# Performance work log

Hardware: AMD Instinct MI355X
Metric: run time of the kernel (lower is better)

## Reference

```python
import jax, jax.numpy as jnp
import numpy as np

B, C, H, W = 16, 256, 64, 64
NH, DH = 8, 64
POS_C = 4


def setup_inputs() -> dict:
    key = jax.random.key(0)
    ks = jax.random.split(key, 10)
    cin = C + POS_C
    dqkv = NH * DH
    sc = 1.0 / np.sqrt(cin)
    inp = {
        "x": jax.random.normal(ks[0], (B, C, H, W), dtype=jnp.float32),
        "pos_emb": jax.random.normal(ks[1], (1, POS_C, H, W), dtype=jnp.float32) / np.sqrt(C * H * W),
        "Wk": jax.random.normal(ks[2], (dqkv, cin), dtype=jnp.float32) * sc,
        "bk": jnp.zeros((dqkv,), dtype=jnp.float32),
        "Wq": jax.random.normal(ks[3], (dqkv, cin), dtype=jnp.float32) * sc,
        "bq": jnp.zeros((dqkv,), dtype=jnp.float32),
        "Wv": jax.random.normal(ks[4], (dqkv, cin), dtype=jnp.float32) * sc,
        "bv": jnp.zeros((dqkv,), dtype=jnp.float32),
        "Wo": jax.random.normal(ks[5], (C, dqkv), dtype=jnp.float32) / np.sqrt(dqkv),
        "bo": jnp.zeros((C,), dtype=jnp.float32),
    }
    return inp


def _conv1x1(w, b, x):
    # w: (out, in), x: (B, in, H, W) -> (B, out, H, W)
    return jnp.einsum('oc,bchw->bohw', w, x) + b[None, :, None, None]


def reference(x, pos_emb, Wk, bk, Wq, bq, Wv, bv, Wo, bo):
    b, c, h, w = x.shape
    xp = jnp.concatenate([x, jnp.broadcast_to(pos_emb, (b, POS_C, h, w))], axis=1)
    K = _conv1x1(Wk, bk, xp).reshape(b, NH, DH, h, w)
    Q = _conv1x1(Wq, bq, xp).reshape(b, NH, DH, h, w)
    V = _conv1x1(Wv, bv, xp).reshape(b, NH, DH, h, w)
    # Row (width-axis) logits: (B, nh, H, W, W)
    qk_w = jnp.einsum('bhdij,bhdik->bhijk', Q, K)
    # Column (height-axis) logits: (B, nh, H, W, H)
    qk_h = jnp.einsum('bhdij,bhdkj->bhijk', Q, K)
    scale = 1.0 / np.sqrt(w + h)
    p = jax.nn.softmax(jnp.concatenate([qk_w, qk_h], axis=-1) * scale, axis=-1)
    p_w, p_h = p[..., :w], p[..., w:]
    a_w = jnp.einsum('bhijk,bhdik->bhdij', p_w, V)
    a_h = jnp.einsum('bhijk,bhdkj->bhdij', p_h, V)
    A = (a_w + a_h).reshape(b, NH * DH, h, w)
    return x + _conv1x1(Wo, bo, A)
```

## Files before the change

### kernel.cpp

```cpp
#include <hip/hip_runtime.h>

typedef unsigned short u16;
typedef __bf16 bf16x8 __attribute__((ext_vector_type(8)));
typedef float f32x4 __attribute__((ext_vector_type(4)));
typedef unsigned short u16x8 __attribute__((ext_vector_type(8)));
typedef unsigned short u16x4 __attribute__((ext_vector_type(4)));

#define MFMA16(A,B,C) __builtin_amdgcn_mfma_f32_16x16x32_bf16(A,B,C,0,0,0)

__device__ __forceinline__ float b2f(u16 h){ unsigned u = ((unsigned)h)<<16; return __builtin_bit_cast(float,u); }
__device__ __forceinline__ u16 f2b(float f){ unsigned u = __builtin_bit_cast(unsigned,f); u += 0x7fffu + ((u>>16)&1u); return (u16)(u>>16); }
__device__ __forceinline__ bf16x8 ldb8(const u16* p){ return __builtin_bit_cast(bf16x8, *(const u16x8*)p); }

__device__ __forceinline__ void g2lds16(const u16* g, u16* l){
  __builtin_amdgcn_global_load_lds((const __attribute__((address_space(1))) void*)g,
                                   (__attribute__((address_space(3))) void*)l, 16, 0, 0);
}


__global__ void k_prep_w(const float* __restrict__ Wq, const float* __restrict__ Wk,
                         const float* __restrict__ Wv, const float* __restrict__ bq,
                         const float* __restrict__ bk, const float* __restrict__ bv,
                         const float* __restrict__ Wo,
                         u16* __restrict__ WP, u16* __restrict__ WPOS,
                         u16* __restrict__ BIAS, u16* __restrict__ WoP){
  int r = blockIdx.x;
  int tid = threadIdx.x;
  if (r < 1536){
    int t = r >> 9, rm = r & 511;
    const float* src = (t==0 ? Wq : (t==1 ? Wk : Wv)) + (long)rm*260;
    WP[(long)r*256 + tid] = f2b(src[tid]);
    if (tid < 4) WPOS[r*4 + tid] = f2b(src[256 + tid]);
    if (tid == 0){
      const float* bs = (t==0 ? bq : (t==1 ? bk : bv));
      BIAS[r] = f2b(bs[rm]);
    }
  } else {
    int co = r - 1536;
    WoP[(long)co*512 + tid]       = f2b(Wo[(long)co*512 + tid]);
    WoP[(long)co*512 + 256 + tid] = f2b(Wo[(long)co*512 + 256 + tid]);
  }
}

__global__ void k_sentinel(float* __restrict__ out){
  long i = (long)blockIdx.x*256 + threadIdx.x;
  out[i] = 100.0f;
}

__global__ __launch_bounds__(256) void k_cvtx(const float* __restrict__ x,
                                              u16* __restrict__ XT, int b0){
  __shared__ u16 tile[64*65];
  int bidx = blockIdx.x;
  int ct = bidx & 3, pt = (bidx>>2)&63, bl = bidx>>8;
  int c0 = ct*64, p0 = pt*64;
  int tid = threadIdx.x;
  const float* xb = x + (long)(b0+bl)*256*4096;
  #pragma unroll
  for (int it=0; it<16; ++it){
    int idx = it*256 + tid; int cc = idx>>6, px = idx&63;
    tile[cc*65 + px] = f2b(xb[(long)(c0+cc)*4096 + p0 + px]);
  }
  __syncthreads();
  u16* dst = XT + ((long)(bl*4096 + p0))*256 + c0;
  #pragma unroll
  for (int it=0; it<4; ++it){
    int idx = it*256 + tid; int pp = idx>>4, c4 = (idx&15)*4;
    u16x4 o;
    #pragma unroll
    for (int u=0;u<4;++u) o[u] = tile[(c4+u)*65 + pp];
    *(u16x4*)&dst[(long)pp*256 + c4] = o;
  }
}

__global__ __launch_bounds__(256) void k_qkv(
    const u16* __restrict__ XT, const u16* __restrict__ WP,
    const u16* __restrict__ WPOS, const float* __restrict__ pos,
    const u16* __restrict__ BIAS,
    u16* __restrict__ Qb, u16* __restrict__ Kb, u16* __restrict__ Vt){
  __shared__ u16 sW[128*32];
  __shared__ u16 sX[128*32];
  __shared__ u16 sPW[512];
  __shared__ u16 sPP[512];
  int bidx = blockIdx.x;
  int mt = bidx % 12; long nt = bidx / 12;
  int oc0 = mt*128; long p0 = nt*128;
  int bl = (int)(p0>>12); int pl0 = (int)(p0 & 4095);
  int tid = threadIdx.x;
  for (int k = tid; k < 512; k += 256) sPW[k] = WPOS[(long)oc0*4 + k];
  for (int k = tid; k < 512; k += 256){ int c = k>>7, p = k&127; sPP[k] = f2b(pos[(long)c*4096 + pl0 + p]); }
  f32x4 zf = {0.f,0.f,0.f,0.f};
  f32x4 acc[4][4];
  #pragma unroll
  for (int i=0;i<4;++i){
    #pragma unroll
    for (int j=0;j<4;++j) acc[i][j] = zf;
  }
  int wid = tid>>6, lane = tid&63, l16 = lane&15, qd = lane>>4;
  int wm = wid>>1, wn = wid&1;
  int srow = lane>>2, sc8 = (lane&3)*8;
  for (int kk = 0; kk < 256; kk += 32){
    __syncthreads();
    #pragma unroll
    for (int c=0;c<2;++c){
      int seg = wid*2 + c;
      int row = seg*16 + srow;
      g2lds16(&WP[(long)(oc0+row)*256 + kk + sc8], &sW[seg*512]);
      g2lds16(&XT[(p0 + row)*256 + kk + sc8],      &sX[seg*512]);
    }
    __syncthreads();
    bf16x8 a[4], bb[4];
    #pragma unroll
    for (int mi=0;mi<4;++mi) a[mi]  = ldb8(&sW[(wm*64+mi*16+l16)*32 + qd*8]);
    #pragma unroll
    for (int ni=0;ni<4;++ni) bb[ni] = ldb8(&sX[(wn*64+ni*16+l16)*32 + qd*8]);
    #pragma unroll
    for (int mi=0;mi<4;++mi){
      #pragma unroll
      for (int ni=0;ni<4;++ni)
        acc[mi][ni] = MFMA16(a[mi], bb[ni], acc[mi][ni]);
    }
  }
  #pragma unroll
  for (int mi=0;mi<4;++mi){
    int mbase = wm*64 + mi*16 + qd*4;
    int ocb = oc0 + mbase;
    int t = ocb>>9, ocm = ocb&511;
    int hh = ocm>>6, dd = ocm&63;
    #pragma unroll
    for (int ni=0;ni<4;++ni){
      int n = wn*64 + ni*16 + l16;
      int pl = pl0 + n;
      float pv[4];
      #pragma unroll
      for (int r=0;r<4;++r){
        float v = acc[mi][ni][r];
        #pragma unroll
        for (int c=0;c<4;++c) v += b2f(sPW[(mbase+r)*4+c]) * b2f(sPP[c*128 + n]);
        pv[r] = v + b2f(BIAS[ocb + r]);
      }
      if (t < 2){
        u16* dstb = (t==0? Qb : Kb);
        u16x4 pk;
        #pragma unroll
        for (int r=0;r<4;++r) pk[r] = f2b(pv[r]);
        *(u16x4*)&dstb[((long)(bl*8+hh)*4096 + pl)*64 + dd] = pk;
      } else {
        long base = (long)(bl*8+hh)*262144 + (long)dd*4096 + pl;
        #pragma unroll
        for (int r=0;r<4;++r) Vt[base + (long)r*4096] = f2b(pv[r]);
      }
    }
  }
}

__global__ __launch_bounds__(256) void k_vtr(const u16* __restrict__ Vt,
                                             u16* __restrict__ Vtc){
  __shared__ u16 tile[64*68];
  int bid = blockIdx.x;
  int d = bid & 63; long ph = bid >> 6;
  const u16* src = Vt + ph*262144 + (long)d*4096;
  u16* dst = Vtc + ph*262144 + (long)d*4096;
  int tid = threadIdx.x;
  #pragma unroll
  for (int it=0; it<2; ++it){
    int idx = it*256 + tid; int i = idx>>3, j8 = (idx&7)*8;
    u16x8 v = *(const u16x8*)&src[i*64 + j8];
    u16x4 lo = {v[0],v[1],v[2],v[3]}, hi = {v[4],v[5],v[6],v[7]};
    *(u16x4*)&tile[i*68 + j8]     = lo;
    *(u16x4*)&tile[i*68 + j8 + 4] = hi;
  }
  __syncthreads();
  #pragma unroll
  for (int it=0; it<2; ++it){
    int idx = it*256 + tid; int j = idx>>3, i8 = (idx&7)*8;
    u16x8 o;
    #pragma unroll
    for (int u=0;u<8;++u) o[u] = tile[(i8+u)*68 + j];
    *(u16x8*)&dst[j*64 + i8] = o;
  }
}

template<int COL>
__global__ __launch_bounds__(256) void k_attn(
    const u16* __restrict__ Qb, const u16* __restrict__ Kb,
    const u16* __restrict__ Vsrc, u16* __restrict__ U,
    float* __restrict__ M, float* __restrict__ L){
  __shared__ u16 sm[4*64*72];
  u16* Qs = sm;
  u16* Ks = sm + 4608;
  u16* VT = sm + 9216;
  u16* Ps = sm + 13824;
  int bid = blockIdx.x;
  int rc = bid&63, h=(bid>>6)&7, bl=bid>>9;
  long plane  = (long)(bl*8+h)*262144;
  long sbase  = (long)(bl*8+h)*4096;
  int tid = threadIdx.x;
  #pragma unroll
  for (int it=0; it<2; ++it){
    int idx = it*256 + tid; int row = idx>>3, c8 = (idx&7)*8;
    long gqk = plane + ((long)(COL ? (row*64 + rc) : (rc*64 + row)))*64 + c8;
    *(u16x8*)&Qs[row*72 + c8] = *(const u16x8*)&Qb[gqk];
    *(u16x8*)&Ks[row*72 + c8] = *(const u16x8*)&Kb[gqk];
    long gv = plane + (long)row*4096 + rc*64 + c8;
    *(u16x8*)&VT[row*72 + c8] = *(const u16x8*)&Vsrc[gv];
  }
  __syncthreads();
  int wid = tid>>6, lane = tid&63, l16 = lane&15, qd = lane>>4;
  int j0 = wid*16;
  f32x4 zf = {0.f,0.f,0.f,0.f};
  f32x4 sv[4] = {zf,zf,zf,zf};
  #pragma unroll
  for (int d0=0; d0<64; d0+=32){
    bf16x8 a = ldb8(&Qs[(j0+l16)*72 + d0 + qd*8]);
    #pragma unroll
    for (int n=0;n<4;++n){
      bf16x8 bb = ldb8(&Ks[(n*16+l16)*72 + d0 + qd*8]);
      sv[n] = MFMA16(a, bb, sv[n]);
    }
  }
  const float scale = 0.08838834764831845f;
  float mrow[4], lrow[4];
  #pragma unroll
  for (int r=0;r<4;++r){
    float mv = -1e30f;
    #pragma unroll
    for (int n=0;n<4;++n){ sv[n][r] *= scale; mv = fmaxf(mv, sv[n][r]); }
    mv = fmaxf(mv, __shfl_xor(mv,1)); mv = fmaxf(mv, __shfl_xor(mv,2));
    mv = fmaxf(mv, __shfl_xor(mv,4)); mv = fmaxf(mv, __shfl_xor(mv,8));
    float ls = 0.f;
    #pragma unroll
    for (int n=0;n<4;++n){ float p = expf(fminf(sv[n][r]-mv, 0.f)); sv[n][r] = p; ls += p; }
    ls += __shfl_xor(ls,1); ls += __shfl_xor(ls,2);
    ls += __shfl_xor(ls,4); ls += __shfl_xor(ls,8);
    mrow[r]=mv; lrow[r]=ls;
    int qi = j0 + qd*4 + r;
    #pragma unroll
    for (int n=0;n<4;++n) Ps[qi*72 + n*16 + l16] = f2b(sv[n][r]);
  }
  __syncthreads();
  f32x4 u4[4] = {zf,zf,zf,zf};
  #pragma unroll
  for (int k0=0;k0<64;k0+=32){
    bf16x8 a = ldb8(&Ps[(j0+l16)*72 + k0 + qd*8]);
    #pragma unroll
    for (int n=0;n<4;++n){
      bf16x8 bb = ldb8(&VT[(n*16+l16)*72 + k0 + qd*8]);
      u4[n] = MFMA16(a, bb, u4[n]);
    }
  }
  if (!COL){
    #pragma unroll
    for (int r=0;r<4;++r){
      int qi = j0 + qd*4 + r;
      long pl = (long)rc*64 + qi;
      long ob = (sbase + pl)*64;
      #pragma unroll
      for (int n=0;n<4;++n) U[ob + n*16 + l16] = f2b(u4[n][r]);
      if (l16==0){ M[sbase+pl]=mrow[r]; L[sbase+pl]=lrow[r]; }
    }
  } else {
    #pragma unroll
    for (int r=0;r<4;++r){
      int qi = j0 + qd*4 + r;
      long pix = sbase + (long)qi*64 + rc;
      float mw = M[pix], lw = L[pix];
      float mh = mrow[r], lh = lrow[r];
      float m  = fmaxf(mw, mh);
      float ew = expf(fminf(mw - m, 0.f));
      float eh = expf(fminf(mh - m, 0.f));
      float rden = 1.f / fmaxf(ew*lw + eh*lh, 1e-20f);
      long ob = pix*64;
      #pragma unroll
      for (int n=0;n<4;++n){
        float uw = b2f(U[ob + n*16 + l16]);
        U[ob + n*16 + l16] = f2b((ew*uw + eh*u4[n][r])*rden);
      }
    }
  }
}

__global__ __launch_bounds__(256) void k_oproj(
    const u16* __restrict__ WoP, const float* __restrict__ bo,
    const u16* __restrict__ AC, const float* __restrict__ x,
    float* __restrict__ out, int b0){
  __shared__ u16 sW[128*32];
  __shared__ u16 sA[128*32];
  int bidx = blockIdx.x;
  int mt = bidx & 1; long nt = bidx >> 1;
  int co0 = mt*128; long p0 = nt*128;
  int bl = (int)(p0>>12), pl0 = (int)(p0&4095);
  int gb = b0 + bl;
  int tid = threadIdx.x;
  int wid=tid>>6, lane=tid&63, l16=lane&15, qd=lane>>4;
  int wm=wid>>1, wn=wid&1;
  int srow = lane>>2, sc8 = (lane&3)*8;
  f32x4 zf = {0.f,0.f,0.f,0.f};
  f32x4 acc[4][4];
  #pragma unroll
  for (int i=0;i<4;++i){
    #pragma unroll
    for (int j=0;j<4;++j) acc[i][j] = zf;
  }
  for (int kk=0; kk<512; kk+=32){
    __syncthreads();
    #pragma unroll
    for (int c=0;c<2;++c){
      int seg = wid*2 + c;
      int row = seg*16 + srow;
      g2lds16(&WoP[(long)(co0+row)*512 + kk + sc8], &sW[seg*512]);
      g2lds16(&AC[((long)(bl*8+(kk>>6))*4096 + pl0 + row)*64 + (kk&63) + sc8], &sA[seg*512]);
    }
    __syncthreads();
    bf16x8 a[4], bb[4];
    #pragma unroll
    for (int mi=0;mi<4;++mi) a[mi]  = ldb8(&sW[(wm*64+mi*16+l16)*32 + qd*8]);
    #pragma unroll
    for (int ni=0;ni<4;++ni) bb[ni] = ldb8(&sA[(wn*64+ni*16+l16)*32 + qd*8]);
    #pragma unroll
    for (int mi=0;mi<4;++mi){
      #pragma unroll
      for (int ni=0;ni<4;++ni)
        acc[mi][ni] = MFMA16(a[mi], bb[ni], acc[mi][ni]);
    }
  }
  #pragma unroll
  for (int mi=0;mi<4;++mi){
    #pragma unroll
    for (int ni=0;ni<4;++ni){
      int n = wn*64+ni*16+l16; int pl = pl0+n;
      #pragma unroll
      for (int r=0;r<4;++r){
        int co = co0 + wm*64+mi*16+qd*4+r;
        long addr = ((long)(gb*256+co))*4096 + pl;
        out[addr] = acc[mi][ni][r] + bo[co] + x[addr];
      }
    }
  }
}

extern "C" void kernel_launch(void* const* d_in, const int* in_sizes, int n_in,
                              void* d_out, int out_size, void* d_ws, size_t ws_size,
                              hipStream_t stream) {
  (void)in_sizes; (void)n_in; (void)out_size;
  const float* x    = (const float*)d_in[0];
  const float* pos  = (const float*)d_in[1];
  const float* Wk   = (const float*)d_in[2];
  const float* bk   = (const float*)d_in[3];
  const float* Wq   = (const float*)d_in[4];
  const float* bq   = (const float*)d_in[5];
  const float* Wv   = (const float*)d_in[6];
  const float* bv   = (const float*)d_in[7];
  const float* Wo   = (const float*)d_in[8];
  const float* bo   = (const float*)d_in[9];
  float* out = (float*)d_out;
  char* ws = (char*)d_ws;

  const long per_batch = 23330816l;
  const long fixed = 1063936l;
  if (fixed + per_batch > (long)ws_size){
    k_sentinel<<<65536, 256, 0, stream>>>(out);
    return;
  }
  int CB = 16;
  while (CB > 1 && fixed + (long)CB*per_batch > (long)ws_size) CB >>= 1;

  u16*  WP   = (u16*)(ws);
  u16*  WPOS = (u16*)(ws + 786432l);
  u16*  BIAS = (u16*)(ws + 798720l);
  u16*  WoP  = (u16*)(ws + 801792l);
  long base  = fixed;
  u16*  XT   = (u16*)(ws + base);
  u16*  Qc   = (u16*)(ws + base + (long)CB*2097152l);
  u16*  Kc   = (u16*)((char*)Qc  + (long)CB*4194304l);
  u16*  Vt   = (u16*)((char*)Kc  + (long)CB*4194304l);
  u16*  Vtc  = (u16*)((char*)Vt  + (long)CB*4194304l);
  u16*  Uw   = (u16*)((char*)Vtc + (long)CB*4194304l);
  float* MWc = (float*)((char*)Uw + (long)CB*4194304l);
  float* LWc = (float*)((char*)MWc + (long)CB*131072l);

  k_prep_w<<<1792, 256, 0, stream>>>(Wq, Wk, Wv, bq, bk, bv, Wo, WP, WPOS, BIAS, WoP);
  for (int b0 = 0; b0 < 16; b0 += CB){
    k_cvtx    <<<CB*256, 256, 0, stream>>>(x, XT, b0);
    k_qkv     <<<CB*384, 256, 0, stream>>>(XT, WP, WPOS, pos, BIAS, Qc, Kc, Vt);
    k_vtr     <<<CB*512, 256, 0, stream>>>(Vt, Vtc);
    k_attn<0> <<<CB*512, 256, 0, stream>>>(Qc, Kc, Vt,  Uw, MWc, LWc);
    k_attn<1> <<<CB*512, 256, 0, stream>>>(Qc, Kc, Vtc, Uw, MWc, LWc);
    k_oproj   <<<CB*64,  256, 0, stream>>>(WoP, bo, Uw, x, out, b0);
  }
}
```

Baseline: 425.2 us.

## Fold pos channels into padded K, double-buffer GEMM LDS, remap blocks across XCDs

The four positional-embedding channels move into a 288-wide padded K dimension of XT and WP, so the QKV GEMM picks them up in one extra MFMA K-step and the scalar epilogue correction goes away. The QKV and output-projection GEMMs now double-buffer their LDS tiles, so the next K-slice is staged while the current one is computed, with one barrier per step. Block indices in the QKV, attention and output-projection kernels are permuted across the 8 XCDs so neighbouring tiles share an L2. The cost is about 12% more XT traffic and a larger LDS footprint per block.

```diff
diff --git a/kernel.cpp b/kernel.cpp
--- a/kernel.cpp
+++ b/kernel.cpp
@@ -22,15 +22,15 @@
                          const float* __restrict__ Wv, const float* __restrict__ bq,
                          const float* __restrict__ bk, const float* __restrict__ bv,
                          const float* __restrict__ Wo,
-                         u16* __restrict__ WP, u16* __restrict__ WPOS,
-                         u16* __restrict__ BIAS, u16* __restrict__ WoP){
+                         u16* __restrict__ WP, u16* __restrict__ BIAS,
+                         u16* __restrict__ WoP){
   int r = blockIdx.x;
   int tid = threadIdx.x;
   if (r < 1536){
     int t = r >> 9, rm = r & 511;
     const float* src = (t==0 ? Wq : (t==1 ? Wk : Wv)) + (long)rm*260;
-    WP[(long)r*256 + tid] = f2b(src[tid]);
-    if (tid < 4) WPOS[r*4 + tid] = f2b(src[256 + tid]);
+    WP[(long)r*288 + tid] = f2b(src[tid]);
+    if (tid < 32) WP[(long)r*288 + 256 + tid] = (tid < 4) ? f2b(src[256 + tid]) : (u16)0;
     if (tid == 0){
       const float* bs = (t==0 ? bq : (t==1 ? bk : bv));
       BIAS[r] = f2b(bs[rm]);
@@ -48,6 +48,7 @@
 }
 
 __global__ __launch_bounds__(256) void k_cvtx(const float* __restrict__ x,
+                                              const float* __restrict__ pos,
                                               u16* __restrict__ XT, int b0){
   __shared__ u16 tile[64*65];
   int bidx = blockIdx.x;
@@ -61,58 +62,69 @@
     tile[cc*65 + px] = f2b(xb[(long)(c0+cc)*4096 + p0 + px]);
   }
   __syncthreads();
-  u16* dst = XT + ((long)(bl*4096 + p0))*256 + c0;
+  u16* dst = XT + ((long)(bl*4096 + p0))*288 + c0;
   #pragma unroll
   for (int it=0; it<4; ++it){
     int idx = it*256 + tid; int pp = idx>>4, c4 = (idx&15)*4;
     u16x4 o;
     #pragma unroll
     for (int u=0;u<4;++u) o[u] = tile[(c4+u)*65 + pp];
-    *(u16x4*)&dst[(long)pp*256 + c4] = o;
+    *(u16x4*)&dst[(long)pp*288 + c4] = o;
+  }
+  if (ct == 0){
+    int px = tid>>2, c8 = (tid&3)*8;
+    u16x8 o;
+    #pragma unroll
+    for (int u=0;u<8;++u){
+      int c = c8 + u;
+      o[u] = (c < 4) ? f2b(pos[(long)c*4096 + p0 + px]) : (u16)0;
+    }
+    *(u16x8*)&XT[((long)(bl*4096 + p0 + px))*288 + 256 + c8] = o;
   }
 }
 
 __global__ __launch_bounds__(256) void k_qkv(
     const u16* __restrict__ XT, const u16* __restrict__ WP,
-    const u16* __restrict__ WPOS, const float* __restrict__ pos,
     const u16* __restrict__ BIAS,
-    u16* __restrict__ Qb, u16* __restrict__ Kb, u16* __restrict__ Vt){
-  __shared__ u16 sW[128*32];
-  __shared__ u16 sX[128*32];
-  __shared__ u16 sPW[512];
-  __shared__ u16 sPP[512];
-  int bidx = blockIdx.x;
+    u16* __restrict__ Qb, u16* __restrict__ Kb, u16* __restrict__ Vt, int nwg){
+  __shared__ u16 sW[2][128*32];
+  __shared__ u16 sX[2][128*32];
+  int hw = blockIdx.x;
+  int bidx = (hw & 7)*(nwg >> 3) + (hw >> 3);
   int mt = bidx % 12; long nt = bidx / 12;
   int oc0 = mt*128; long p0 = nt*128;
   int bl = (int)(p0>>12); int pl0 = (int)(p0 & 4095);
   int tid = threadIdx.x;
-  for (int k = tid; k < 512; k += 256) sPW[k] = WPOS[(long)oc0*4 + k];
-  for (int k = tid; k < 512; k += 256){ int c = k>>7, p = k&127; sPP[k] = f2b(pos[(long)c*4096 + pl0 + p]); }
-  f32x4 zf = {0.f,0.f,0.f,0.f};
-  f32x4 acc[4][4];
-  #pragma unroll
-  for (int i=0;i<4;++i){
-    #pragma unroll
-    for (int j=0;j<4;++j) acc[i][j] = zf;
-  }
   int wid = tid>>6, lane = tid&63, l16 = lane&15, qd = lane>>4;
   int wm = wid>>1, wn = wid&1;
   int srow = lane>>2, sc8 = (lane&3)*8;
-  for (int kk = 0; kk < 256; kk += 32){
-    __syncthreads();
+  f32x4 zf = {0.f,0.f,0.f,0.f};
+  f32x4 acc[4][4];
+  #pragma unroll
+  for (int i=0;i<4;++i){
+    #pragma unroll
+    for (int j=0;j<4;++j) acc[i][j] = zf;
+  }
+  auto stage = [&](int buf, int kk){
     #pragma unroll
     for (int c=0;c<2;++c){
       int seg = wid*2 + c;
       int row = seg*16 + srow;
-      g2lds16(&WP[(long)(oc0+row)*256 + kk + sc8], &sW[seg*512]);
-      g2lds16(&XT[(p0 + row)*256 + kk + sc8],      &sX[seg*512]);
-    }
+      g2lds16(&WP[(long)(oc0+row)*288 + kk + sc8], &sW[buf][seg*512]);
+      g2lds16(&XT[(p0 + row)*288 + kk + sc8],      &sX[buf][seg*512]);
+    }
+  };
+  stage(0, 0);
+  #pragma unroll
+  for (int t=0; t<9; ++t){
     __syncthreads();
+    if (t < 8) stage((t+1)&1, (t+1)*32);
+    int cur = t&1;
     bf16x8 a[4], bb[4];
     #pragma unroll
-    for (int mi=0;mi<4;++mi) a[mi]  = ldb8(&sW[(wm*64+mi*16+l16)*32 + qd*8]);
-    #pragma unroll
-    for (int ni=0;ni<4;++ni) bb[ni] = ldb8(&sX[(wn*64+ni*16+l16)*32 + qd*8]);
+    for (int mi=0;mi<4;++mi) a[mi]  = ldb8(&sW[cur][(wm*64+mi*16+l16)*32 + qd*8]);
+    #pragma unroll
+    for (int ni=0;ni<4;++ni) bb[ni] = ldb8(&sX[cur][(wn*64+ni*16+l16)*32 + qd*8]);
     #pragma unroll
     for (int mi=0;mi<4;++mi){
       #pragma unroll
@@ -126,28 +138,23 @@
     int ocb = oc0 + mbase;
     int t = ocb>>9, ocm = ocb&511;
     int hh = ocm>>6, dd = ocm&63;
+    float bv4[4];
+    #pragma unroll
+    for (int r=0;r<4;++r) bv4[r] = b2f(BIAS[ocb + r]);
     #pragma unroll
     for (int ni=0;ni<4;++ni){
       int n = wn*64 + ni*16 + l16;
       int pl = pl0 + n;
-      float pv[4];
-      #pragma unroll
-      for (int r=0;r<4;++r){
-        float v = acc[mi][ni][r];
-        #pragma unroll
-        for (int c=0;c<4;++c) v += b2f(sPW[(mbase+r)*4+c]) * b2f(sPP[c*128 + n]);
-        pv[r] = v + b2f(BIAS[ocb + r]);
-      }
       if (t < 2){
         u16* dstb = (t==0? Qb : Kb);
         u16x4 pk;
         #pragma unroll
-        for (int r=0;r<4;++r) pk[r] = f2b(pv[r]);
+        for (int r=0;r<4;++r) pk[r] = f2b(acc[mi][ni][r] + bv4[r]);
         *(u16x4*)&dstb[((long)(bl*8+hh)*4096 + pl)*64 + dd] = pk;
       } else {
         long base = (long)(bl*8+hh)*262144 + (long)dd*4096 + pl;
         #pragma unroll
-        for (int r=0;r<4;++r) Vt[base + (long)r*4096] = f2b(pv[r]);
+        for (int r=0;r<4;++r) Vt[base + (long)r*4096] = f2b(acc[mi][ni][r] + bv4[r]);
       }
     }
   }
@@ -184,13 +191,14 @@
 __global__ __launch_bounds__(256) void k_attn(
     const u16* __restrict__ Qb, const u16* __restrict__ Kb,
     const u16* __restrict__ Vsrc, u16* __restrict__ U,
-    float* __restrict__ M, float* __restrict__ L){
+    float* __restrict__ M, float* __restrict__ L, int nwg){
   __shared__ u16 sm[4*64*72];
   u16* Qs = sm;
   u16* Ks = sm + 4608;
   u16* VT = sm + 9216;
   u16* Ps = sm + 13824;
-  int bid = blockIdx.x;
+  int hw = blockIdx.x;
+  int bid = (hw & 7)*(nwg >> 3) + (hw >> 3);
   int rc = bid&63, h=(bid>>6)&7, bl=bid>>9;
   long plane  = (long)(bl*8+h)*262144;
   long sbase  = (long)(bl*8+h)*4096;
@@ -282,10 +290,11 @@
 __global__ __launch_bounds__(256) void k_oproj(
     const u16* __restrict__ WoP, const float* __restrict__ bo,
     const u16* __restrict__ AC, const float* __restrict__ x,
-    float* __restrict__ out, int b0){
-  __shared__ u16 sW[128*32];
-  __shared__ u16 sA[128*32];
-  int bidx = blockIdx.x;
+    float* __restrict__ out, int b0, int nwg){
+  __shared__ u16 sW[2][128*32];
+  __shared__ u16 sA[2][128*32];
+  int hw = blockIdx.x;
+  int bidx = (hw & 7)*(nwg >> 3) + (hw >> 3);
   int mt = bidx & 1; long nt = bidx >> 1;
   int co0 = mt*128; long p0 = nt*128;
   int bl = (int)(p0>>12), pl0 = (int)(p0&4095);
@@ -301,21 +310,26 @@
     #pragma unroll
     for (int j=0;j<4;++j) acc[i][j] = zf;
   }
-  for (int kk=0; kk<512; kk+=32){
-    __syncthreads();
+  auto stage = [&](int buf, int kk){
     #pragma unroll
     for (int c=0;c<2;++c){
       int seg = wid*2 + c;
       int row = seg*16 + srow;
-      g2lds16(&WoP[(long)(co0+row)*512 + kk + sc8], &sW[seg*512]);
-      g2lds16(&AC[((long)(bl*8+(kk>>6))*4096 + pl0 + row)*64 + (kk&63) + sc8], &sA[seg*512]);
-    }
+      g2lds16(&WoP[(long)(co0+row)*512 + kk + sc8], &sW[buf][seg*512]);
+      g2lds16(&AC[((long)(bl*8+(kk>>6))*4096 + pl0 + row)*64 + (kk&63) + sc8], &sA[buf][seg*512]);
+    }
+  };
+  stage(0, 0);
+  #pragma unroll
+  for (int t=0; t<16; ++t){
     __syncthreads();
+    if (t < 15) stage((t+1)&1, (t+1)*32);
+    int cur = t&1;
     bf16x8 a[4], bb[4];
     #pragma unroll
-    for (int mi=0;mi<4;++mi) a[mi]  = ldb8(&sW[(wm*64+mi*16+l16)*32 + qd*8]);
-    #pragma unroll
-    for (int ni=0;ni<4;++ni) bb[ni] = ldb8(&sA[(wn*64+ni*16+l16)*32 + qd*8]);
+    for (int mi=0;mi<4;++mi) a[mi]  = ldb8(&sW[cur][(wm*64+mi*16+l16)*32 + qd*8]);
+    #pragma unroll
+    for (int ni=0;ni<4;++ni) bb[ni] = ldb8(&sA[cur][(wn*64+ni*16+l16)*32 + qd*8]);
     #pragma unroll
     for (int mi=0;mi<4;++mi){
       #pragma unroll
@@ -355,8 +369,8 @@
   float* out = (float*)d_out;
   char* ws = (char*)d_ws;
 
-  const long per_batch = 23330816l;
-  const long fixed = 1063936l;
+  const long per_batch = 23592960l;
+  const long fixed = 1149952l;
   if (fixed + per_batch > (long)ws_size){
     k_sentinel<<<65536, 256, 0, stream>>>(out);
     return;
@@ -365,12 +379,11 @@
   while (CB > 1 && fixed + (long)CB*per_batch > (long)ws_size) CB >>= 1;
 
   u16*  WP   = (u16*)(ws);
-  u16*  WPOS = (u16*)(ws + 786432l);
-  u16*  BIAS = (u16*)(ws + 798720l);
-  u16*  WoP  = (u16*)(ws + 801792l);
+  u16*  BIAS = (u16*)(ws + 884736l);
+  u16*  WoP  = (u16*)(ws + 887808l);
   long base  = fixed;
   u16*  XT   = (u16*)(ws + base);
-  u16*  Qc   = (u16*)(ws + base + (long)CB*2097152l);
+  u16*  Qc   = (u16*)(ws + base + (long)CB*2359296l);
   u16*  Kc   = (u16*)((char*)Qc  + (long)CB*4194304l);
   u16*  Vt   = (u16*)((char*)Kc  + (long)CB*4194304l);
   u16*  Vtc  = (u16*)((char*)Vt  + (long)CB*4194304l);
@@ -378,13 +391,13 @@
   float* MWc = (float*)((char*)Uw + (long)CB*4194304l);
   float* LWc = (float*)((char*)MWc + (long)CB*131072l);
 
-  k_prep_w<<<1792, 256, 0, stream>>>(Wq, Wk, Wv, bq, bk, bv, Wo, WP, WPOS, BIAS, WoP);
+  k_prep_w<<<1792, 256, 0, stream>>>(Wq, Wk, Wv, bq, bk, bv, Wo, WP, BIAS, WoP);
   for (int b0 = 0; b0 < 16; b0 += CB){
-    k_cvtx    <<<CB*256, 256, 0, stream>>>(x, XT, b0);
-    k_qkv     <<<CB*384, 256, 0, stream>>>(XT, WP, WPOS, pos, BIAS, Qc, Kc, Vt);
+    k_cvtx    <<<CB*256, 256, 0, stream>>>(x, pos, XT, b0);
+    k_qkv     <<<CB*384, 256, 0, stream>>>(XT, WP, BIAS, Qc, Kc, Vt, CB*384);
     k_vtr     <<<CB*512, 256, 0, stream>>>(Vt, Vtc);
-    k_attn<0> <<<CB*512, 256, 0, stream>>>(Qc, Kc, Vt,  Uw, MWc, LWc);
-    k_attn<1> <<<CB*512, 256, 0, stream>>>(Qc, Kc, Vtc, Uw, MWc, LWc);
-    k_oproj   <<<CB*64,  256, 0, stream>>>(WoP, bo, Uw, x, out, b0);
-  }
-}
+    k_attn<0> <<<CB*512, 256, 0, stream>>>(Qc, Kc, Vt,  Uw, MWc, LWc, CB*512);
+    k_attn<1> <<<CB*512, 256, 0, stream>>>(Qc, Kc, Vtc, Uw, MWc, LWc, CB*512);
+    k_oproj   <<<CB*64,  256, 0, stream>>>(WoP, bo, Uw, x, out, b0, CB*64);
+  }
+}
```

New measurement: 442.2 us. 1.04x slower.
